# Optimization experiments

Measured on AMD Instinct MI355X. Metric: run time of the kernel, lower is better.

Reference implementation:

```python
import jax, jax.numpy as jnp
import numpy as np

EPS = 1e-6
DROP_RATE = 0.25

def setup_inputs() -> dict:
    key = jax.random.key(0)
    k1, k2, k3 = jax.random.split(key, 3)
    B, S, D = 4, 2048, 2048
    inputs = jax.random.normal(k1, (B, S, D), dtype=jnp.float32)
    # keras 'uniform' initializer: U(-0.05, 0.05)
    W_1 = jax.random.uniform(k2, (D, D), dtype=jnp.float32, minval=-0.05, maxval=0.05)
    W_2 = jax.random.uniform(k3, (D, D), dtype=jnp.float32, minval=-0.05, maxval=0.05)
    return {"inputs": inputs, "W_1": W_1, "W_2": W_2}

def reference(inputs, W_1, W_2):
    # LayerNorm over last axis (no affine: gamma/beta unused in original call)
    mean = jnp.mean(inputs, axis=-1, keepdims=True)
    var = jnp.mean(jnp.square(inputs - mean), axis=-1, keepdims=True)
    x_norm = (inputs - mean) / jnp.sqrt(var + EPS)          # [B,S,D]
    # 2-layer MLP with relu
    h = jax.nn.relu(jnp.einsum('bsd,de->bse', x_norm, W_1))  # [B,S,D]
    y = jnp.einsum('bsd,de->bse', h, W_2)                    # [B,S,D]
    # dropout(0.25), inverted scaling, fixed key for determinism
    keep = jax.random.bernoulli(jax.random.key(1), 1.0 - DROP_RATE, y.shape)
    y_drop = jnp.where(keep, y / (1.0 - DROP_RATE), 0.0)
    return x_norm + y_drop
```

## Files before the change

### kernel.cpp

```cpp
#include <hip/hip_runtime.h>
#include <hip/hip_bf16.h>
#include <stdint.h>

#define M_DIM 8192
#define N_DIM 2048
#define K_DIM 2048

typedef __bf16 bf16x8_t __attribute__((ext_vector_type(8)));
typedef float f32x4_t __attribute__((ext_vector_type(4)));

__device__ __forceinline__ unsigned tf_rotl(unsigned x, int r) {
  return (x << r) | (x >> (32 - r));
}
__device__ __forceinline__ unsigned threefry_mask_bits(unsigned ctr) {
  unsigned x0 = 0u, x1 = ctr;
  const unsigned ks0 = 0u, ks1 = 1u, ks2 = 0x1BD11BDBu;
  x0 += ks0; x1 += ks1;
#define TFR(r) { x0 += x1; x1 = tf_rotl(x1, (r)); x1 ^= x0; }
  TFR(13) TFR(15) TFR(26) TFR(6)
  x0 += ks1; x1 += ks2 + 1u;
  TFR(17) TFR(29) TFR(16) TFR(24)
  x0 += ks2; x1 += ks0 + 2u;
  TFR(13) TFR(15) TFR(26) TFR(6)
  x0 += ks0; x1 += ks1 + 3u;
  TFR(17) TFR(29) TFR(16) TFR(24)
  x0 += ks1; x1 += ks2 + 4u;
  TFR(13) TFR(15) TFR(26) TFR(6)
  x0 += ks2; x1 += ks0 + 5u;
#undef TFR
  return x0 ^ x1;
}

__device__ __forceinline__ void gload_lds16(const __hip_bfloat16* g, unsigned short* l) {
  __builtin_amdgcn_global_load_lds(
      (const __attribute__((address_space(1))) unsigned int*)g,
      (__attribute__((address_space(3))) unsigned int*)l,
      16, 0, 0);
}

__global__ __launch_bounds__(256) void wt_kernel(
    const float* __restrict__ W1, const float* __restrict__ W2,
    __hip_bfloat16* __restrict__ W1t, __hip_bfloat16* __restrict__ W2t) {
  __shared__ float tile[32][33];
  const float* src = blockIdx.z ? W2 : W1;
  __hip_bfloat16* dst = blockIdx.z ? W2t : W1t;
  int x = blockIdx.x * 32 + threadIdx.x;
  int y = blockIdx.y * 32 + threadIdx.y;
#pragma unroll
  for (int i = 0; i < 32; i += 8)
    tile[threadIdx.y + i][threadIdx.x] = src[(size_t)(y + i) * N_DIM + x];
  __syncthreads();
  int xo = blockIdx.y * 32 + threadIdx.x;
  int yo = blockIdx.x * 32 + threadIdx.y;
#pragma unroll
  for (int i = 0; i < 32; i += 8)
    dst[(size_t)(yo + i) * K_DIM + xo] = __float2bfloat16(tile[threadIdx.x][threadIdx.y + i]);
}

__global__ __launch_bounds__(256) void ln_kernel(const float* __restrict__ X,
                                                 __hip_bfloat16* __restrict__ Xn) {
  const int row = blockIdx.x;
  const float4* xv = (const float4*)(X + (size_t)row * K_DIM);
  float4 v0 = xv[threadIdx.x];
  float4 v1 = xv[threadIdx.x + 256];
  float s  = v0.x + v0.y + v0.z + v0.w + v1.x + v1.y + v1.z + v1.w;
  float ss = v0.x*v0.x + v0.y*v0.y + v0.z*v0.z + v0.w*v0.w
           + v1.x*v1.x + v1.y*v1.y + v1.z*v1.z + v1.w*v1.w;
#pragma unroll
  for (int off = 32; off > 0; off >>= 1) {
    s  += __shfl_xor(s, off);
    ss += __shfl_xor(ss, off);
  }
  __shared__ float rs[4], rss[4];
  const int wave = threadIdx.x >> 6;
  if ((threadIdx.x & 63) == 0) { rs[wave] = s; rss[wave] = ss; }
  __syncthreads();
  float S  = rs[0] + rs[1] + rs[2] + rs[3];
  float SS = rss[0] + rss[1] + rss[2] + rss[3];
  float mean = S * (1.0f / 2048.0f);
  float var  = SS * (1.0f / 2048.0f) - mean * mean;
  float rstd = 1.0f / sqrtf(var + 1e-6f);
  float vv[8] = {v0.x, v0.y, v0.z, v0.w, v1.x, v1.y, v1.z, v1.w};
  unsigned short o[8];
#pragma unroll
  for (int i = 0; i < 8; i++) {
    __hip_bfloat16 b = __float2bfloat16((vv[i] - mean) * rstd);
    o[i] = *(unsigned short*)&b;
  }
  ushort4* dst = (ushort4*)(Xn + (size_t)row * K_DIM);
  dst[threadIdx.x]       = make_ushort4(o[0], o[1], o[2], o[3]);
  dst[threadIdx.x + 256] = make_ushort4(o[4], o[5], o[6], o[7]);
}

template <int EPI>
__global__ __launch_bounds__(256) void gemm128(
    const __hip_bfloat16* __restrict__ A,
    const __hip_bfloat16* __restrict__ Bt,
    const __hip_bfloat16* __restrict__ Xn,
    __hip_bfloat16* __restrict__ Hout,
    float* __restrict__ Fout) {
  __shared__ unsigned short As[128 * 32];
  __shared__ unsigned short Bs[128 * 32];
  const int tid  = threadIdx.x;
  const int lane = tid & 63;
  const int wave = tid >> 6;
  const int wm = wave >> 1, wn = wave & 1;
  const int mBase = blockIdx.y * 128;
  const int nBase = blockIdx.x * 128;

  f32x4_t acc[4][4];
#pragma unroll
  for (int i = 0; i < 4; i++)
#pragma unroll
    for (int j = 0; j < 4; j++) acc[i][j] = (f32x4_t){0.f, 0.f, 0.f, 0.f};

  const int r4 = lane >> 2;
  const int c4 = (lane & 3) << 3;
  const __hip_bfloat16* a0 = A  + (size_t)(mBase + 16 * wave       + r4) * K_DIM + c4;
  const __hip_bfloat16* a1 = A  + (size_t)(mBase + 16 * (wave + 4) + r4) * K_DIM + c4;
  const __hip_bfloat16* b0 = Bt + (size_t)(nBase + 16 * wave       + r4) * K_DIM + c4;
  const __hip_bfloat16* b1 = Bt + (size_t)(nBase + 16 * (wave + 4) + r4) * K_DIM + c4;
  unsigned short* asDst0 = &As[(16 * wave) * 32];
  unsigned short* asDst1 = &As[(16 * (wave + 4)) * 32];
  unsigned short* bsDst0 = &Bs[(16 * wave) * 32];
  unsigned short* bsDst1 = &Bs[(16 * (wave + 4)) * 32];

  const int fr = lane & 15;
  const int fq = lane >> 4;
  const unsigned short* aRead = &As[(wm * 64 + fr) * 32 + fq * 8];
  const unsigned short* bRead = &Bs[(wn * 64 + fr) * 32 + fq * 8];

  for (int k0 = 0; k0 < K_DIM; k0 += 32) {
    gload_lds16(a0 + k0, asDst0);
    gload_lds16(a1 + k0, asDst1);
    gload_lds16(b0 + k0, bsDst0);
    gload_lds16(b1 + k0, bsDst1);
    __syncthreads();
    bf16x8_t af[4], bfr[4];
#pragma unroll
    for (int i = 0; i < 4; i++) af[i]  = *(const bf16x8_t*)(aRead + i * 16 * 32);
#pragma unroll
    for (int i = 0; i < 4; i++) bfr[i] = *(const bf16x8_t*)(bRead + i * 16 * 32);
#pragma unroll
    for (int mi = 0; mi < 4; mi++)
#pragma unroll
      for (int ni = 0; ni < 4; ni++)
        acc[mi][ni] = __builtin_amdgcn_mfma_f32_16x16x32_bf16(af[mi], bfr[ni], acc[mi][ni], 0, 0, 0);
    __syncthreads();
  }

  const int mRow = mBase + wm * 64;
  const int nCol = nBase + wn * 64;
#pragma unroll
  for (int mi = 0; mi < 4; mi++) {
#pragma unroll
    for (int ni = 0; ni < 4; ni++) {
      const int n  = nCol + ni * 16 + fr;
      const int m0 = mRow + mi * 16 + fq * 4;
#pragma unroll
      for (int r = 0; r < 4; r++) {
        float v = acc[mi][ni][r];
        size_t j = (size_t)(m0 + r) * N_DIM + n;
        if (EPI == 0) {
          Hout[j] = __float2bfloat16(fmaxf(v, 0.0f));
        } else {
          unsigned bits = threefry_mask_bits((unsigned)j);
          float y  = (bits < 0xC0000000u) ? v * (1.0f / 0.75f) : 0.0f;
          Fout[j]  = __bfloat162float(Xn[j]) + y;
        }
      }
    }
  }
}

extern "C" void kernel_launch(void* const* d_in, const int* in_sizes, int n_in,
                              void* d_out, int out_size, void* d_ws, size_t ws_size,
                              hipStream_t stream) {
  (void)in_sizes; (void)n_in; (void)out_size; (void)ws_size;
  const float* X  = (const float*)d_in[0];
  const float* W1 = (const float*)d_in[1];
  const float* W2 = (const float*)d_in[2];
  float* out = (float*)d_out;

  unsigned char* ws = (unsigned char*)d_ws;
  __hip_bfloat16* Xn  = (__hip_bfloat16*)(ws);
  __hip_bfloat16* H   = (__hip_bfloat16*)(ws + ((size_t)32 << 20));
  __hip_bfloat16* W1t = (__hip_bfloat16*)(ws + ((size_t)64 << 20));
  __hip_bfloat16* W2t = (__hip_bfloat16*)(ws + ((size_t)72 << 20));

  wt_kernel<<<dim3(64, 64, 2), dim3(32, 8, 1), 0, stream>>>(W1, W2, W1t, W2t);
  ln_kernel<<<M_DIM, 256, 0, stream>>>(X, Xn);
  gemm128<0><<<dim3(N_DIM / 128, M_DIM / 128), 256, 0, stream>>>(Xn, W1t, nullptr, H, nullptr);
  gemm128<1><<<dim3(N_DIM / 128, M_DIM / 128), 256, 0, stream>>>(H, W2t, Xn, nullptr, out);
}
```

Baseline: 353.1 us.

## Double-buffer LDS tiles in GEMM and swap grid rasterization order

The GEMM main loop now uses two LDS buffers for the A and B tiles. The global-to-LDS loads for the next K-slice are issued before the MFMA work on the current slice, so memory latency can overlap with compute. The grid is also transposed so that blockIdx.x walks along M instead of N, which changes which tiles neighbouring blocks share in L2. LDS use per block doubles, which may reduce occupancy, and each barrier still waits for the outstanding prefetch.

```diff
diff --git a/kernel.cpp b/kernel.cpp
--- a/kernel.cpp
+++ b/kernel.cpp
@@ -99,14 +99,14 @@
     const __hip_bfloat16* __restrict__ Xn,
     __hip_bfloat16* __restrict__ Hout,
     float* __restrict__ Fout) {
-  __shared__ unsigned short As[128 * 32];
-  __shared__ unsigned short Bs[128 * 32];
+  __shared__ unsigned short As[2][128 * 32];
+  __shared__ unsigned short Bs[2][128 * 32];
   const int tid  = threadIdx.x;
   const int lane = tid & 63;
   const int wave = tid >> 6;
   const int wm = wave >> 1, wn = wave & 1;
-  const int mBase = blockIdx.y * 128;
-  const int nBase = blockIdx.x * 128;
+  const int mBase = blockIdx.x * 128;
+  const int nBase = blockIdx.y * 128;
 
   f32x4_t acc[4][4];
 #pragma unroll
@@ -120,34 +120,47 @@
   const __hip_bfloat16* a1 = A  + (size_t)(mBase + 16 * (wave + 4) + r4) * K_DIM + c4;
   const __hip_bfloat16* b0 = Bt + (size_t)(nBase + 16 * wave       + r4) * K_DIM + c4;
   const __hip_bfloat16* b1 = Bt + (size_t)(nBase + 16 * (wave + 4) + r4) * K_DIM + c4;
-  unsigned short* asDst0 = &As[(16 * wave) * 32];
-  unsigned short* asDst1 = &As[(16 * (wave + 4)) * 32];
-  unsigned short* bsDst0 = &Bs[(16 * wave) * 32];
-  unsigned short* bsDst1 = &Bs[(16 * (wave + 4)) * 32];
+  const int sOff0 = (16 * wave) * 32;
+  const int sOff1 = (16 * (wave + 4)) * 32;
 
   const int fr = lane & 15;
   const int fq = lane >> 4;
-  const unsigned short* aRead = &As[(wm * 64 + fr) * 32 + fq * 8];
-  const unsigned short* bRead = &Bs[(wn * 64 + fr) * 32 + fq * 8];
-
-  for (int k0 = 0; k0 < K_DIM; k0 += 32) {
-    gload_lds16(a0 + k0, asDst0);
-    gload_lds16(a1 + k0, asDst1);
-    gload_lds16(b0 + k0, bsDst0);
-    gload_lds16(b1 + k0, bsDst1);
+  const int rdOffA = (wm * 64 + fr) * 32 + fq * 8;
+  const int rdOffB = (wn * 64 + fr) * 32 + fq * 8;
+
+#define STAGE(buf, k0)                              \
+  {                                                 \
+    gload_lds16(a0 + (k0), &As[buf][sOff0]);        \
+    gload_lds16(a1 + (k0), &As[buf][sOff1]);        \
+    gload_lds16(b0 + (k0), &Bs[buf][sOff0]);        \
+    gload_lds16(b1 + (k0), &Bs[buf][sOff1]);        \
+  }
+
+#define COMPUTE(buf)                                                            \
+  {                                                                             \
+    bf16x8_t af[4], bfr[4];                                                     \
+    _Pragma("unroll")                                                           \
+    for (int i = 0; i < 4; i++) af[i]  = *(const bf16x8_t*)(&As[buf][rdOffA] + i * 16 * 32); \
+    _Pragma("unroll")                                                           \
+    for (int i = 0; i < 4; i++) bfr[i] = *(const bf16x8_t*)(&Bs[buf][rdOffB] + i * 16 * 32); \
+    _Pragma("unroll")                                                           \
+    for (int mi = 0; mi < 4; mi++)                                              \
+      _Pragma("unroll")                                                         \
+      for (int ni = 0; ni < 4; ni++)                                            \
+        acc[mi][ni] = __builtin_amdgcn_mfma_f32_16x16x32_bf16(af[mi], bfr[ni], acc[mi][ni], 0, 0, 0); \
+  }
+
+  STAGE(0, 0)
+  for (int k0 = 0; k0 < K_DIM; k0 += 64) {
     __syncthreads();
-    bf16x8_t af[4], bfr[4];
-#pragma unroll
-    for (int i = 0; i < 4; i++) af[i]  = *(const bf16x8_t*)(aRead + i * 16 * 32);
-#pragma unroll
-    for (int i = 0; i < 4; i++) bfr[i] = *(const bf16x8_t*)(bRead + i * 16 * 32);
-#pragma unroll
-    for (int mi = 0; mi < 4; mi++)
-#pragma unroll
-      for (int ni = 0; ni < 4; ni++)
-        acc[mi][ni] = __builtin_amdgcn_mfma_f32_16x16x32_bf16(af[mi], bfr[ni], acc[mi][ni], 0, 0, 0);
+    if (k0 + 32 < K_DIM) STAGE(1, k0 + 32)
+    COMPUTE(0)
     __syncthreads();
-  }
+    if (k0 + 64 < K_DIM) STAGE(0, k0 + 64)
+    COMPUTE(1)
+  }
+#undef STAGE
+#undef COMPUTE
 
   const int mRow = mBase + wm * 64;
   const int nCol = nBase + wn * 64;
@@ -190,6 +203,6 @@
 
   wt_kernel<<<dim3(64, 64, 2), dim3(32, 8, 1), 0, stream>>>(W1, W2, W1t, W2t);
   ln_kernel<<<M_DIM, 256, 0, stream>>>(X, Xn);
-  gemm128<0><<<dim3(N_DIM / 128, M_DIM / 128), 256, 0, stream>>>(Xn, W1t, nullptr, H, nullptr);
-  gemm128<1><<<dim3(N_DIM / 128, M_DIM / 128), 256, 0, stream>>>(H, W2t, Xn, nullptr, out);
-}
+  gemm128<0><<<dim3(M_DIM / 128, N_DIM / 128), 256, 0, stream>>>(Xn, W1t, nullptr, H, nullptr);
+  gemm128<1><<<dim3(M_DIM / 128, N_DIM / 128), 256, 0, stream>>>(H, W2t, Xn, nullptr, out);
+}
```

Measured after the change: 363.1 us. +2.8%, slower.
